# Kernel optimization log

Hardware: AMD Instinct MI355X
Metric: run time of the kernel (lower is better)

The kernel has to match this reference:

```python
import jax, jax.numpy as jnp
import numpy as np

B, L, E = 128, 512, 128
NUM_Q, NUM_C, DIFF = 10000, 300, 100


def _lin(k, fan_in, fan_out):
    kw, kb = jax.random.split(k)
    s = 1.0 / np.sqrt(fan_in)
    W = jax.random.uniform(kw, (fan_in, fan_out), jnp.float32, -s, s)
    b = jax.random.uniform(kb, (fan_out,), jnp.float32, -s, s)
    return W, b


def setup_inputs() -> dict:
    key = jax.random.key(0)
    ks = jax.random.split(key, 24)
    inp = {
        "q": jax.random.randint(ks[0], (B, L), 0, NUM_Q),
        "c": jax.random.randint(ks[1], (B, L), 0, NUM_C),
        "sd": jax.random.randint(ks[2], (B, L), 0, DIFF + 99),
        "qd": jax.random.randint(ks[3], (B, L), 0, DIFF + 99),
        "a": jax.random.randint(ks[4], (B, L), 0, 2 * NUM_Q + 1),
        "qshft": jax.random.randint(ks[5], (B, L), 0, NUM_Q),
        "cshft": jax.random.randint(ks[6], (B, L), 0, NUM_C),
        "sdshft": jax.random.randint(ks[7], (B, L), 0, DIFF + 99),
        "qdshft": jax.random.randint(ks[8], (B, L), 0, DIFF + 99),
        "knowledge": jax.random.normal(ks[9], (1, E), jnp.float32) * 0.1,
        "q_tab": jax.random.normal(ks[10], (NUM_Q + 1, E), jnp.float32),
        "c_tab": jax.random.normal(ks[11], (NUM_C + 1, E), jnp.float32),
        "sd_tab": jax.random.normal(ks[12], (DIFF + 100, E), jnp.float32),
        "qd_tab": jax.random.normal(ks[13], (DIFF + 100, E), jnp.float32),
        "a_tab": jax.random.normal(ks[14], (2 * NUM_Q + 2, E), jnp.float32),
    }
    for name, fan_in, ki in [("1", 4 * E, 15), ("2", E, 16), ("3", E, 17),
                             ("4", 2 * E, 18), ("5", 2 * E, 19), ("6", 4 * E, 20)]:
        W, b = _lin(ks[ki], fan_in, E)
        inp[f"W{name}"], inp[f"b{name}"] = W, b
    Wf, bf = _lin(ks[21], E, 10)
    inp["Wf"], inp["bf"] = Wf, bf
    return inp


def reference(q, c, sd, qd, a, qshft, cshft, sdshft, qdshft,
              knowledge, q_tab, c_tab, sd_tab, qd_tab, a_tab,
              W1, b1, W2, b2, W3, b3, W4, b4, W5, b5, W6, b6, Wf, bf):
    # Embedding lookups  [B, L, E]
    q_e, c_e = q_tab[q], c_tab[c]
    sd_e, qd_e = sd_tab[sd], qd_tab[qd]
    a_e = a_tab[a]
    # input_data = linear_1(cat(q,c,sd,qd))  [B, L, E]
    inp = jnp.concatenate([q_e, c_e, sd_e, qd_e], -1) @ W1 + b1
    # (target_data in the torch code is dead: never used for the output)

    k0 = jnp.broadcast_to(knowledge, (q.shape[0], knowledge.shape[1]))  # [B, E]

    def step(k, xs):
        x, sd1, a1, qd1 = xs  # each [B, E]
        qq = x - k
        SDFt = jax.nn.sigmoid(qq @ W2 + b2) * jnp.tanh(qq @ W3 + b3)  # dropout=eval
        xa = jnp.concatenate([SDFt, a1], -1)
        PKAt = jax.nn.sigmoid(xa @ W4 + b4) * jnp.tanh(xa @ W5 + b5)
        ins = jnp.concatenate([k, a1, sd1, qd1], -1)
        gK = jax.nn.sigmoid(ins @ W6 + b6)
        k_new = gK * k + (1.0 - gK) * PKAt
        return k_new, k_new @ Wf + bf

    xs = (jnp.swapaxes(inp, 0, 1), jnp.swapaxes(sd_e, 0, 1),
          jnp.swapaxes(a_e, 0, 1), jnp.swapaxes(qd_e, 0, 1))  # [L, B, E]
    _, logits = jax.lax.scan(step, k0, xs)  # [L, B, 10]
    return jax.nn.sigmoid(jnp.swapaxes(logits, 0, 1))  # [B, L, 10]
```

## Files before the change

### kernel.cpp

```cpp
#include <hip/hip_runtime.h>
#include <hip/hip_bf16.h>
#include <stdint.h>

#define E_DIM 128
#define L_SEQ 512
#define B_SZ  128

typedef _Float16 h2 __attribute__((ext_vector_type(2)));
typedef _Float16 f16x8 __attribute__((ext_vector_type(8)));
typedef float f32x4 __attribute__((ext_vector_type(4)));

constexpr size_t SZ_W12 = 512 * 128 * 4;
constexpr size_t SZ_TQ  = 10001 * 128 * 4;
constexpr size_t SZ_TC  = 301 * 128 * 4;
constexpr size_t SZ_TS  = 200 * 128 * 4;
constexpr size_t SZ_TA  = 20002 * 128 * 4;

constexpr size_t OFF_W12  = 0;
constexpr size_t OFF_W13  = OFF_W12 + SZ_W12;
constexpr size_t OFF_BV2  = OFF_W13 + SZ_W12;
constexpr size_t OFF_BV3  = OFF_BV2 + 512;
constexpr size_t OFF_TQ2  = OFF_BV3 + 512;
constexpr size_t OFF_TQ3  = OFF_TQ2 + SZ_TQ;
constexpr size_t OFF_TC2  = OFF_TQ3 + SZ_TQ;
constexpr size_t OFF_TC3  = OFF_TC2 + SZ_TC;
constexpr size_t OFF_TSD2 = OFF_TC3 + SZ_TC;
constexpr size_t OFF_TSD3 = OFF_TSD2 + SZ_TS;
constexpr size_t OFF_TSD6 = OFF_TSD3 + SZ_TS;
constexpr size_t OFF_TQD2 = OFF_TSD6 + SZ_TS;
constexpr size_t OFF_TQD3 = OFF_TQD2 + SZ_TS;
constexpr size_t OFF_TQD6 = OFF_TQD3 + SZ_TS;
constexpr size_t OFF_TA4  = OFF_TQD6 + SZ_TS;
constexpr size_t OFF_TA5  = OFF_TA4 + SZ_TA;
constexpr size_t OFF_TA6  = OFF_TA5 + SZ_TA;
constexpr size_t OFF_K    = OFF_TA6 + SZ_TA;

__device__ __forceinline__ float fdot2f(unsigned int a, unsigned int b, float c) {
#if __has_builtin(__builtin_amdgcn_fdot2)
  return __builtin_amdgcn_fdot2(__builtin_bit_cast(h2, a), __builtin_bit_cast(h2, b), c, false);
#else
  h2 x = __builtin_bit_cast(h2, a), y = __builtin_bit_cast(h2, b);
  return c + (float)x[0] * (float)y[0] + (float)x[1] * (float)y[1];
#endif
}

__device__ __forceinline__ unsigned int packh2(float a, float b) {
  h2 v; v[0] = (_Float16)a; v[1] = (_Float16)b;
  return __builtin_bit_cast(unsigned int, v);
}

__device__ __forceinline__ float fsig(float x) {
  float t = __builtin_amdgcn_exp2f(-1.4426950408889634f * x);
  return __builtin_amdgcn_rcpf(1.0f + t);
}
__device__ __forceinline__ float ftanh(float x) {
  float t = __builtin_amdgcn_exp2f(2.8853900817779268f * x);
  return 1.0f - 2.0f * __builtin_amdgcn_rcpf(t + 1.0f);
}

#define BARRIER_RAW() asm volatile("s_waitcnt lgkmcnt(0)\n\ts_barrier" ::: "memory")

__global__ __launch_bounds__(256, 2) void prepA_kernel(
    const float* __restrict__ W1, const float* __restrict__ W2, const float* __restrict__ W3,
    const float* __restrict__ b1, const float* __restrict__ b2, const float* __restrict__ b3,
    char* __restrict__ ws) {
  float* W12 = (float*)(ws + OFF_W12);
  float* W13 = (float*)(ws + OFF_W13);
  float* bv2 = (float*)(ws + OFF_BV2);
  float* bv3 = (float*)(ws + OFF_BV3);
  const int blk = blockIdx.x, tid = threadIdx.x;
  if (blk < 512) {
    const int m = blk >> 8;
    const int rp = blk & 255;
    const float* M = m ? W3 : W2;
    float* dst = m ? W13 : W12;
    const int rr = tid >> 7, j = tid & 127;
    const int r = rp * 2 + rr;
    __shared__ float rowL[2][128];
    rowL[rr][j] = W1[r * 128 + j];
    __syncthreads();
    float acc = 0.0f;
#pragma unroll 8
    for (int t = 0; t < 128; t++) acc += rowL[rr][t] * M[t * 128 + j];
    dst[r * 128 + j] = acc;
  } else if (tid < 128) {
    float a2 = b2[tid], a3 = b3[tid];
    for (int t = 0; t < 128; t++) {
      float bb = b1[t];
      a2 += bb * W2[t * 128 + tid];
      a3 += bb * W3[t * 128 + tid];
    }
    bv2[tid] = a2;
    bv3[tid] = a3;
  }
}

__global__ __launch_bounds__(256, 2) void gemm_tab1_kernel(
    const float* __restrict__ q_tab, const float* __restrict__ c_tab,
    const float* __restrict__ sd_tab, const float* __restrict__ qd_tab,
    const float* __restrict__ a_tab,
    const float* __restrict__ W4, const float* __restrict__ W5, const float* __restrict__ W6,
    const float* __restrict__ b4, const float* __restrict__ b5, const float* __restrict__ b6,
    char* __restrict__ ws) {
  __shared__ _Float16 BT[128][136];
  __shared__ _Float16 At[32][136];
  __shared__ float biasL[128];

  const float* W12 = (const float*)(ws + OFF_W12);
  const float* W13 = (const float*)(ws + OFF_W13);
  const float* bv2f = (const float*)(ws + OFF_BV2);
  const float* bv3f = (const float*)(ws + OFF_BV3);

  const int bid = blockIdx.x, tid = threadIdx.x;
  const int wv = tid >> 6, ln = tid & 63;

  int task, rb;
  if      (bid < 79)  { task = 0;  rb = bid; }
  else if (bid < 158) { task = 1;  rb = bid - 79; }
  else if (bid < 161) { task = 2;  rb = bid - 158; }
  else if (bid < 164) { task = 3;  rb = bid - 161; }
  else if (bid < 166) { task = 4;  rb = bid - 164; }
  else if (bid < 168) { task = 5;  rb = bid - 166; }
  else if (bid < 170) { task = 6;  rb = bid - 168; }
  else if (bid < 172) { task = 7;  rb = bid - 170; }
  else if (bid < 174) { task = 8;  rb = bid - 172; }
  else if (bid < 176) { task = 9;  rb = bid - 174; }
  else if (bid < 333) { task = 10; rb = bid - 176; }
  else if (bid < 490) { task = 11; rb = bid - 333; }
  else                { task = 12; rb = bid - 490; }

  const float* src; int rows; const float* Bsrc; const float* bias; float* dst;
  switch (task) {
    case 0:  src = q_tab;  rows = 10001; Bsrc = W12;            bias = bv2f;   dst = (float*)(ws + OFF_TQ2);  break;
    case 1:  src = q_tab;  rows = 10001; Bsrc = W13;            bias = bv3f;   dst = (float*)(ws + OFF_TQ3);  break;
    case 2:  src = c_tab;  rows = 301;   Bsrc = W12 + 128*128;  bias = nullptr; dst = (float*)(ws + OFF_TC2);  break;
    case 3:  src = c_tab;  rows = 301;   Bsrc = W13 + 128*128;  bias = nullptr; dst = (float*)(ws + OFF_TC3);  break;
    case 4:  src = sd_tab; rows = 200;   Bsrc = W12 + 256*128;  bias = nullptr; dst = (float*)(ws + OFF_TSD2); break;
    case 5:  src = sd_tab; rows = 200;   Bsrc = W13 + 256*128;  bias = nullptr; dst = (float*)(ws + OFF_TSD3); break;
    case 6:  src = sd_tab; rows = 200;   Bsrc = W6  + 256*128;  bias = nullptr; dst = (float*)(ws + OFF_TSD6); break;
    case 7:  src = qd_tab; rows = 200;   Bsrc = W12 + 384*128;  bias = nullptr; dst = (float*)(ws + OFF_TQD2); break;
    case 8:  src = qd_tab; rows = 200;   Bsrc = W13 + 384*128;  bias = nullptr; dst = (float*)(ws + OFF_TQD3); break;
    case 9:  src = qd_tab; rows = 200;   Bsrc = W6  + 384*128;  bias = nullptr; dst = (float*)(ws + OFF_TQD6); break;
    case 10: src = a_tab;  rows = 20002; Bsrc = W4  + 128*128;  bias = b4;     dst = (float*)(ws + OFF_TA4);  break;
    case 11: src = a_tab;  rows = 20002; Bsrc = W5  + 128*128;  bias = b5;     dst = (float*)(ws + OFF_TA5);  break;
    default: src = a_tab;  rows = 20002; Bsrc = W6  + 128*128;  bias = b6;     dst = (float*)(ws + OFF_TA6);  break;
  }

#pragma unroll
  for (int r = 0; r < 8; r++) {
    const int k = (tid >> 4) + r * 16;
    const int j0 = (tid & 15) * 8;
    float4 v0 = *(const float4*)(Bsrc + k * 128 + j0);
    float4 v1 = *(const float4*)(Bsrc + k * 128 + j0 + 4);
    BT[j0 + 0][k] = (_Float16)v0.x; BT[j0 + 1][k] = (_Float16)v0.y;
    BT[j0 + 2][k] = (_Float16)v0.z; BT[j0 + 3][k] = (_Float16)v0.w;
    BT[j0 + 4][k] = (_Float16)v1.x; BT[j0 + 5][k] = (_Float16)v1.y;
    BT[j0 + 6][k] = (_Float16)v1.z; BT[j0 + 7][k] = (_Float16)v1.w;
  }
  if (tid < 128) biasL[tid] = bias ? bias[tid] : 0.0f;
  __syncthreads();

  f16x8 bfr[2][4];
#pragma unroll
  for (int ct = 0; ct < 2; ct++)
#pragma unroll
    for (int kt = 0; kt < 4; kt++) {
      const int col = wv * 32 + ct * 16 + (ln & 15);
      const int k = kt * 32 + (ln >> 4) * 8;
      bfr[ct][kt] = *(const f16x8*)&BT[col][k];
    }
  float bvl[2] = { biasL[wv * 32 + (ln & 15)], biasL[wv * 32 + 16 + (ln & 15)] };

  const int row_base = rb * 128;
  for (int ch = 0; ch < 4; ch++) {
    const int row0 = row_base + ch * 32;
    {
      const int r = tid >> 3, cb = (tid & 7) * 16;
      int sr = row0 + r; if (sr >= rows) sr = rows - 1;
      const float4* s4 = (const float4*)(src + (size_t)sr * 128 + cb);
      float4 v0 = s4[0], v1 = s4[1], v2 = s4[2], v3 = s4[3];
      f16x8 lo, hi;
      lo[0] = (_Float16)v0.x; lo[1] = (_Float16)v0.y; lo[2] = (_Float16)v0.z; lo[3] = (_Float16)v0.w;
      lo[4] = (_Float16)v1.x; lo[5] = (_Float16)v1.y; lo[6] = (_Float16)v1.z; lo[7] = (_Float16)v1.w;
      hi[0] = (_Float16)v2.x; hi[1] = (_Float16)v2.y; hi[2] = (_Float16)v2.z; hi[3] = (_Float16)v2.w;
      hi[4] = (_Float16)v3.x; hi[5] = (_Float16)v3.y; hi[6] = (_Float16)v3.z; hi[7] = (_Float16)v3.w;
      *(f16x8*)&At[r][cb] = lo;
      *(f16x8*)&At[r][cb + 8] = hi;
    }
    __syncthreads();
    f16x8 af[2][4];
#pragma unroll
    for (int rt = 0; rt < 2; rt++)
#pragma unroll
      for (int kt = 0; kt < 4; kt++) {
        const int row = rt * 16 + (ln & 15);
        const int k = kt * 32 + (ln >> 4) * 8;
        af[rt][kt] = *(const f16x8*)&At[row][k];
      }
    f32x4 acc[2][2];
#pragma unroll
    for (int rt = 0; rt < 2; rt++)
#pragma unroll
      for (int ct = 0; ct < 2; ct++) acc[rt][ct] = (f32x4){0.f, 0.f, 0.f, 0.f};
#pragma unroll
    for (int kt = 0; kt < 4; kt++)
#pragma unroll
      for (int ct = 0; ct < 2; ct++)
#pragma unroll
        for (int rt = 0; rt < 2; rt++)
          acc[rt][ct] = __builtin_amdgcn_mfma_f32_16x16x32_f16(af[rt][kt], bfr[ct][kt], acc[rt][ct], 0, 0, 0);
#pragma unroll
    for (int ct = 0; ct < 2; ct++) {
      const int col = wv * 32 + ct * 16 + (ln & 15);
      const float bv = bvl[ct];
#pragma unroll
      for (int rt = 0; rt < 2; rt++)
#pragma unroll
        for (int e = 0; e < 4; e++) {
          const int row = row0 + rt * 16 + (ln >> 4) * 4 + e;
          if (row < rows) dst[(size_t)row * 128 + col] = acc[rt][ct][e] + bv;
        }
    }
    __syncthreads();
  }
}


#define PREFETCH(S, P) do {                                                   \
    int _s = (S);                                                             \
    int _qi = idxb[g][0][_s], _ci = idxb[g][1][_s], _si = idxb[g][2][_s];     \
    int _di = idxb[g][3][_s], _ai = idxb[g][4][_s];                           \
    P##q2 = Tq2[_qi * 128 + j]; P##q3 = Tq3[_qi * 128 + j];                   \
    P##c2 = Tc2[_ci * 128 + j]; P##c3 = Tc3[_ci * 128 + j];                   \
    P##s2 = Ts2[_si * 128 + j]; P##s3 = Ts3[_si * 128 + j];                   \
    P##s6 = Ts6[_si * 128 + j];                                               \
    P##d2 = Td2[_di * 128 + j]; P##d3 = Td3[_di * 128 + j];                   \
    P##d6 = Td6[_di * 128 + j];                                               \
    P##a4 = Ta4[_ai * 128 + j]; P##a5 = Ta5[_ai * 128 + j];                   \
    P##a6 = Ta6[_ai * 128 + j];                                               \
  } while (0)

#define SCAN_STEP(P, S2, L) do {                                              \
    float u2a = 0.f, u2b = 0.f, u3a = 0.f, u3b = 0.f, u6a = 0.f, u6b = 0.f;   \
    {                                                                         \
      const uint4* kp4 = ((const uint4*)kpair[g]) + 8 * h;                    \
      _Pragma("unroll")                                                       \
      for (int i = 0; i < 8; i++) {                                           \
        uint4 kv = kp4[i];                                                    \
        u2a = fdot2f(kv.x, w2h[4 * i + 0], u2a);                              \
        u3a = fdot2f(kv.x, w3h[4 * i + 0], u3a);                              \
        u6a = fdot2f(kv.x, w6h[4 * i + 0], u6a);                              \
        u2b = fdot2f(kv.y, w2h[4 * i + 1], u2b);                              \
        u3b = fdot2f(kv.y, w3h[4 * i + 1], u3b);                              \
        u6b = fdot2f(kv.y, w6h[4 * i + 1], u6b);                              \
        u2a = fdot2f(kv.z, w2h[4 * i + 2], u2a);                              \
        u3a = fdot2f(kv.z, w3h[4 * i + 2], u3a);                              \
        u6a = fdot2f(kv.z, w6h[4 * i + 2], u6a);                              \
        u2b = fdot2f(kv.w, w2h[4 * i + 3], u2b);                              \
        u3b = fdot2f(kv.w, w3h[4 * i + 3], u3b);                              \
        u6b = fdot2f(kv.w, w6h[4 * i + 3], u6b);                              \
      }                                                                       \
    }                                                                         \
    float U2p = u2a + u2b, U3p = u3a + u3b, U6p = u6a + u6b;                  \
    U2p += __shfl_xor(U2p, 32);                                               \
    U3p += __shfl_xor(U3p, 32);                                               \
    U6p += __shfl_xor(U6p, 32);                                               \
    float U2 = (P##q2 + P##c2 + P##s2 + P##d2) - U2p;                         \
    float U3 = (P##q3 + P##c3 + P##s3 + P##d3) - U3p;                         \
    float U6 = (P##a6 + P##s6 + P##d6) + U6p;                                 \
    float sdft = fsig(U2) * ftanh(U3);                                        \
    float g_ = fsig(U6);                                                      \
    if (!h) ((_Float16*)sdfp[g])[j] = (_Float16)sdft;                         \
    BARRIER_RAW();                                    \
    float u4a = 0.f, u4b = 0.f, u5a = 0.f, u5b = 0.f;                         \
    {                                                                         \
      const uint4* sp4 = ((const uint4*)sdfp[g]) + 8 * h;                     \
      _Pragma("unroll")                                                       \
      for (int i = 0; i < 8; i++) {                                           \
        uint4 sv = sp4[i];                                                    \
        u4a = fdot2f(sv.x, w4h[4 * i + 0], u4a);                              \
        u5a = fdot2f(sv.x, w5h[4 * i + 0], u5a);                              \
        u4b = fdot2f(sv.y, w4h[4 * i + 1], u4b);                              \
        u5b = fdot2f(sv.y, w5h[4 * i + 1], u5b);                              \
        u4a = fdot2f(sv.z, w4h[4 * i + 2], u4a);                              \
        u5a = fdot2f(sv.z, w5h[4 * i + 2], u5a);                              \
        u4b = fdot2f(sv.w, w4h[4 * i + 3], u4b);                              \
        u5b = fdot2f(sv.w, w5h[4 * i + 3], u5b);                              \
      }                                                                       \
    }                                                                         \
    float U4p = u4a + u4b, U5p = u5a + u5b;                                   \
    U4p += __shfl_xor(U4p, 32);                                               \
    U5p += __shfl_xor(U5p, 32);                                               \
    float pk = fsig(U4p + P##a4) * ftanh(U5p + P##a5);                        \
    k = g_ * k + (1.0f - g_) * pk;                                            \
    if (h) ((_Float16*)kpair[g])[j] = (_Float16)k;                            \
    if (!h) Kout[((size_t)(base + (L))) * 128 + j] = k;                       \
    PREFETCH(S2, P);                                                          \
    BARRIER_RAW();                                       \
  } while (0)

__global__ __launch_bounds__(512, 2) void scan_kernel(
    const int* __restrict__ q, const int* __restrict__ c, const int* __restrict__ sd,
    const int* __restrict__ qd, const int* __restrict__ a,
    const float* __restrict__ knowledge,
    const float* __restrict__ W2, const float* __restrict__ W3, const float* __restrict__ W4,
    const float* __restrict__ W5, const float* __restrict__ W6,
    char* __restrict__ ws) {
  const int tid = threadIdx.x;
  const int g = tid >> 8;
  const int t256 = tid & 255;
  const int ln = tid & 63;
  const int wvl = (t256 >> 6);
  const int j = (wvl << 5) | (ln & 31);
  const int h = ln >> 5;
  const int b = (blockIdx.x << 1) | g;
  const int base = b * L_SEQ;

  const float* Tq2 = (const float*)(ws + OFF_TQ2);
  const float* Tq3 = (const float*)(ws + OFF_TQ3);
  const float* Tc2 = (const float*)(ws + OFF_TC2);
  const float* Tc3 = (const float*)(ws + OFF_TC3);
  const float* Ts2 = (const float*)(ws + OFF_TSD2);
  const float* Ts3 = (const float*)(ws + OFF_TSD3);
  const float* Ts6 = (const float*)(ws + OFF_TSD6);
  const float* Td2 = (const float*)(ws + OFF_TQD2);
  const float* Td3 = (const float*)(ws + OFF_TQD3);
  const float* Td6 = (const float*)(ws + OFF_TQD6);
  const float* Ta4 = (const float*)(ws + OFF_TA4);
  const float* Ta5 = (const float*)(ws + OFF_TA5);
  const float* Ta6 = (const float*)(ws + OFF_TA6);
  float* Kout = (float*)(ws + OFF_K);

  __shared__ int idxb[2][5][L_SEQ];
  __shared__ __align__(16) unsigned int kpair[2][64];
  __shared__ __align__(16) unsigned int sdfp[2][64];

  idxb[g][0][t256] = q[base + t256];  idxb[g][0][t256 + 256] = q[base + t256 + 256];
  idxb[g][1][t256] = c[base + t256];  idxb[g][1][t256 + 256] = c[base + t256 + 256];
  idxb[g][2][t256] = sd[base + t256]; idxb[g][2][t256 + 256] = sd[base + t256 + 256];
  idxb[g][3][t256] = qd[base + t256]; idxb[g][3][t256 + 256] = qd[base + t256 + 256];
  idxb[g][4][t256] = a[base + t256];  idxb[g][4][t256 + 256] = a[base + t256 + 256];

  unsigned int w2h[32], w3h[32], w6h[32], w4h[32], w5h[32];
  const int t0 = h * 64;
#pragma unroll
  for (int p = 0; p < 32; p++) {
    w2h[p] = packh2(W2[(t0 + 2 * p) * 128 + j], W2[(t0 + 2 * p + 1) * 128 + j]);
    w3h[p] = packh2(W3[(t0 + 2 * p) * 128 + j], W3[(t0 + 2 * p + 1) * 128 + j]);
    w6h[p] = packh2(W6[(t0 + 2 * p) * 128 + j], W6[(t0 + 2 * p + 1) * 128 + j]);
    w4h[p] = packh2(W4[(t0 + 2 * p) * 128 + j], W4[(t0 + 2 * p + 1) * 128 + j]);
    w5h[p] = packh2(W5[(t0 + 2 * p) * 128 + j], W5[(t0 + 2 * p + 1) * 128 + j]);
  }

  float k = knowledge[j];
  if (h) ((_Float16*)kpair[g])[j] = (_Float16)k;
  __syncthreads();

  float gAq2, gAq3, gAc2, gAc3, gAs2, gAs3, gAs6, gAd2, gAd3, gAd6, gAa4, gAa5, gAa6;
  float gBq2, gBq3, gBc2, gBc3, gBs2, gBs3, gBs6, gBd2, gBd3, gBd6, gBa4, gBa5, gBa6;
  PREFETCH(0, gA);
  PREFETCH(1, gB);

#pragma unroll 1
  for (int m = 0; m < L_SEQ / 2; m++) {
    const int l0 = 2 * m;
    const int s2 = (l0 + 2 < L_SEQ) ? (l0 + 2) : (L_SEQ - 1);
    const int s3 = (l0 + 3 < L_SEQ) ? (l0 + 3) : (L_SEQ - 1);
    SCAN_STEP(gA, s2, l0);
    SCAN_STEP(gB, s3, l0 + 1);
  }
}

__global__ __launch_bounds__(256, 2) void logits_kernel(
    const float* __restrict__ Wf, const float* __restrict__ bf,
    const char* __restrict__ ws, float* __restrict__ out) {
  __shared__ float WfL[1280];
  __shared__ float bfL[10];
  const int tid = threadIdx.x;
  for (int i = tid; i < 1280; i += 256) WfL[i] = Wf[i];
  if (tid < 10) bfL[tid] = bf[tid];
  __syncthreads();
  const float* K = (const float*)(ws + OFF_K);
  const int nrows = B_SZ * L_SEQ;
  for (int r = blockIdx.x * 256 + tid; r < nrows; r += gridDim.x * 256) {
    const float4* kr = (const float4*)(K + (size_t)r * 128);
    float acc[10];
#pragma unroll
    for (int i = 0; i < 10; i++) acc[i] = bfL[i];
#pragma unroll
    for (int t4 = 0; t4 < 32; t4++) {
      float4 v = kr[t4];
#pragma unroll
      for (int i = 0; i < 10; i++)
        acc[i] += v.x * WfL[(4 * t4 + 0) * 10 + i] + v.y * WfL[(4 * t4 + 1) * 10 + i] +
                  v.z * WfL[(4 * t4 + 2) * 10 + i] + v.w * WfL[(4 * t4 + 3) * 10 + i];
    }
    float* o = out + (size_t)r * 10;
#pragma unroll
    for (int i = 0; i < 10; i++) o[i] = fsig(acc[i]);
  }
}

extern "C" void kernel_launch(void* const* d_in, const int* in_sizes, int n_in,
                              void* d_out, int out_size, void* d_ws, size_t ws_size,
                              hipStream_t stream) {
  const int* q  = (const int*)d_in[0];
  const int* c  = (const int*)d_in[1];
  const int* sd = (const int*)d_in[2];
  const int* qd = (const int*)d_in[3];
  const int* a  = (const int*)d_in[4];
  const float* knowledge = (const float*)d_in[9];
  const float* q_tab  = (const float*)d_in[10];
  const float* c_tab  = (const float*)d_in[11];
  const float* sd_tab = (const float*)d_in[12];
  const float* qd_tab = (const float*)d_in[13];
  const float* a_tab  = (const float*)d_in[14];
  const float* W1 = (const float*)d_in[15];
  const float* b1 = (const float*)d_in[16];
  const float* W2 = (const float*)d_in[17];
  const float* b2 = (const float*)d_in[18];
  const float* W3 = (const float*)d_in[19];
  const float* b3 = (const float*)d_in[20];
  const float* W4 = (const float*)d_in[21];
  const float* b4 = (const float*)d_in[22];
  const float* W5 = (const float*)d_in[23];
  const float* b5 = (const float*)d_in[24];
  const float* W6 = (const float*)d_in[25];
  const float* b6 = (const float*)d_in[26];
  const float* Wf = (const float*)d_in[27];
  const float* bf = (const float*)d_in[28];
  char* ws = (char*)d_ws;
  float* out = (float*)d_out;

  prepA_kernel<<<513, 256, 0, stream>>>(W1, W2, W3, b1, b2, b3, ws);
  gemm_tab1_kernel<<<647, 256, 0, stream>>>(q_tab, c_tab, sd_tab, qd_tab, a_tab,
                                            W4, W5, W6, b4, b5, b6, ws);
  scan_kernel<<<B_SZ / 2, 512, 0, stream>>>(q, c, sd, qd, a, knowledge, W2, W3, W4, W5, W6, ws);
  logits_kernel<<<256, 256, 0, stream>>>(Wf, bf, ws, out);
}
```

Measured before the change: 883.6 us.

## Interleave precomputed projection tables for vector gathers in scan

The precomputed per-embedding projection tables are now written interleaved (q/c pairs, sd/qd quads, a4/a5 pairs), so each scan step issues six vector gathers instead of thirteen scalar loads. Gather indices are made wave-uniform with readfirstlane so the address math can live in scalar registers. The scan kernel's launch bounds drop to one block per SM, which gives the compiler more registers but may lower occupancy. The precompute stores become strided, which could cost some write efficiency.

New measurement: 888.2 us. No clear change (+0.5%).

```diff
diff --git a/kernel.cpp b/kernel.cpp
--- a/kernel.cpp
+++ b/kernel.cpp
@@ -10,30 +10,26 @@
 typedef _Float16 f16x8 __attribute__((ext_vector_type(8)));
 typedef float f32x4 __attribute__((ext_vector_type(4)));
 
-constexpr size_t SZ_W12 = 512 * 128 * 4;
-constexpr size_t SZ_TQ  = 10001 * 128 * 4;
-constexpr size_t SZ_TC  = 301 * 128 * 4;
-constexpr size_t SZ_TS  = 200 * 128 * 4;
-constexpr size_t SZ_TA  = 20002 * 128 * 4;
+constexpr size_t SZ_W12  = 512 * 128 * 4;
+constexpr size_t SZ_TQ   = (size_t)10001 * 128 * 2 * 4;
+constexpr size_t SZ_TC   = (size_t)301 * 128 * 2 * 4;
+constexpr size_t SZ_TSD  = (size_t)200 * 128 * 4 * 4;
+constexpr size_t SZ_TQD  = (size_t)200 * 128 * 4 * 4;
+constexpr size_t SZ_TA45 = (size_t)20002 * 128 * 2 * 4;
+constexpr size_t SZ_TA6  = (size_t)20002 * 128 * 4;
+constexpr size_t SZ_K    = (size_t)B_SZ * L_SEQ * 128 * 4;
 
 constexpr size_t OFF_W12  = 0;
 constexpr size_t OFF_W13  = OFF_W12 + SZ_W12;
 constexpr size_t OFF_BV2  = OFF_W13 + SZ_W12;
 constexpr size_t OFF_BV3  = OFF_BV2 + 512;
-constexpr size_t OFF_TQ2  = OFF_BV3 + 512;
-constexpr size_t OFF_TQ3  = OFF_TQ2 + SZ_TQ;
-constexpr size_t OFF_TC2  = OFF_TQ3 + SZ_TQ;
-constexpr size_t OFF_TC3  = OFF_TC2 + SZ_TC;
-constexpr size_t OFF_TSD2 = OFF_TC3 + SZ_TC;
-constexpr size_t OFF_TSD3 = OFF_TSD2 + SZ_TS;
-constexpr size_t OFF_TSD6 = OFF_TSD3 + SZ_TS;
-constexpr size_t OFF_TQD2 = OFF_TSD6 + SZ_TS;
-constexpr size_t OFF_TQD3 = OFF_TQD2 + SZ_TS;
-constexpr size_t OFF_TQD6 = OFF_TQD3 + SZ_TS;
-constexpr size_t OFF_TA4  = OFF_TQD6 + SZ_TS;
-constexpr size_t OFF_TA5  = OFF_TA4 + SZ_TA;
-constexpr size_t OFF_TA6  = OFF_TA5 + SZ_TA;
-constexpr size_t OFF_K    = OFF_TA6 + SZ_TA;
+constexpr size_t OFF_TQ   = OFF_BV3 + 512;
+constexpr size_t OFF_TC   = OFF_TQ + SZ_TQ;
+constexpr size_t OFF_TSD  = OFF_TC + SZ_TC;
+constexpr size_t OFF_TQD  = OFF_TSD + SZ_TSD;
+constexpr size_t OFF_TA45 = OFF_TQD + SZ_TQD;
+constexpr size_t OFF_TA6  = OFF_TA45 + SZ_TA45;
+constexpr size_t OFF_K    = OFF_TA6 + SZ_TA6;
 
 __device__ __forceinline__ float fdot2f(unsigned int a, unsigned int b, float c) {
 #if __has_builtin(__builtin_amdgcn_fdot2)
@@ -129,21 +125,22 @@
   else if (bid < 490) { task = 11; rb = bid - 333; }
   else                { task = 12; rb = bid - 490; }
 
-  const float* src; int rows; const float* Bsrc; const float* bias; float* dst;
+  const float* src; int rows; const float* Bsrc; const float* bias;
+  float* dst; int STR, ILV, SLOT;
   switch (task) {
-    case 0:  src = q_tab;  rows = 10001; Bsrc = W12;            bias = bv2f;   dst = (float*)(ws + OFF_TQ2);  break;
-    case 1:  src = q_tab;  rows = 10001; Bsrc = W13;            bias = bv3f;   dst = (float*)(ws + OFF_TQ3);  break;
-    case 2:  src = c_tab;  rows = 301;   Bsrc = W12 + 128*128;  bias = nullptr; dst = (float*)(ws + OFF_TC2);  break;
-    case 3:  src = c_tab;  rows = 301;   Bsrc = W13 + 128*128;  bias = nullptr; dst = (float*)(ws + OFF_TC3);  break;
-    case 4:  src = sd_tab; rows = 200;   Bsrc = W12 + 256*128;  bias = nullptr; dst = (float*)(ws + OFF_TSD2); break;
-    case 5:  src = sd_tab; rows = 200;   Bsrc = W13 + 256*128;  bias = nullptr; dst = (float*)(ws + OFF_TSD3); break;
-    case 6:  src = sd_tab; rows = 200;   Bsrc = W6  + 256*128;  bias = nullptr; dst = (float*)(ws + OFF_TSD6); break;
-    case 7:  src = qd_tab; rows = 200;   Bsrc = W12 + 384*128;  bias = nullptr; dst = (float*)(ws + OFF_TQD2); break;
-    case 8:  src = qd_tab; rows = 200;   Bsrc = W13 + 384*128;  bias = nullptr; dst = (float*)(ws + OFF_TQD3); break;
-    case 9:  src = qd_tab; rows = 200;   Bsrc = W6  + 384*128;  bias = nullptr; dst = (float*)(ws + OFF_TQD6); break;
-    case 10: src = a_tab;  rows = 20002; Bsrc = W4  + 128*128;  bias = b4;     dst = (float*)(ws + OFF_TA4);  break;
-    case 11: src = a_tab;  rows = 20002; Bsrc = W5  + 128*128;  bias = b5;     dst = (float*)(ws + OFF_TA5);  break;
-    default: src = a_tab;  rows = 20002; Bsrc = W6  + 128*128;  bias = b6;     dst = (float*)(ws + OFF_TA6);  break;
+    case 0:  src = q_tab;  rows = 10001; Bsrc = W12;           bias = bv2f;    dst = (float*)(ws + OFF_TQ);   STR = 256; ILV = 2; SLOT = 0; break;
+    case 1:  src = q_tab;  rows = 10001; Bsrc = W13;           bias = bv3f;    dst = (float*)(ws + OFF_TQ);   STR = 256; ILV = 2; SLOT = 1; break;
+    case 2:  src = c_tab;  rows = 301;   Bsrc = W12 + 128*128; bias = nullptr; dst = (float*)(ws + OFF_TC);   STR = 256; ILV = 2; SLOT = 0; break;
+    case 3:  src = c_tab;  rows = 301;   Bsrc = W13 + 128*128; bias = nullptr; dst = (float*)(ws + OFF_TC);   STR = 256; ILV = 2; SLOT = 1; break;
+    case 4:  src = sd_tab; rows = 200;   Bsrc = W12 + 256*128; bias = nullptr; dst = (float*)(ws + OFF_TSD);  STR = 512; ILV = 4; SLOT = 0; break;
+    case 5:  src = sd_tab; rows = 200;   Bsrc = W13 + 256*128; bias = nullptr; dst = (float*)(ws + OFF_TSD);  STR = 512; ILV = 4; SLOT = 1; break;
+    case 6:  src = sd_tab; rows = 200;   Bsrc = W6  + 256*128; bias = nullptr; dst = (float*)(ws + OFF_TSD);  STR = 512; ILV = 4; SLOT = 2; break;
+    case 7:  src = qd_tab; rows = 200;   Bsrc = W12 + 384*128; bias = nullptr; dst = (float*)(ws + OFF_TQD);  STR = 512; ILV = 4; SLOT = 0; break;
+    case 8:  src = qd_tab; rows = 200;   Bsrc = W13 + 384*128; bias = nullptr; dst = (float*)(ws + OFF_TQD);  STR = 512; ILV = 4; SLOT = 1; break;
+    case 9:  src = qd_tab; rows = 200;   Bsrc = W6  + 384*128; bias = nullptr; dst = (float*)(ws + OFF_TQD);  STR = 512; ILV = 4; SLOT = 2; break;
+    case 10: src = a_tab;  rows = 20002; Bsrc = W4  + 128*128; bias = b4;      dst = (float*)(ws + OFF_TA45); STR = 256; ILV = 2; SLOT = 0; break;
+    case 11: src = a_tab;  rows = 20002; Bsrc = W5  + 128*128; bias = b5;      dst = (float*)(ws + OFF_TA45); STR = 256; ILV = 2; SLOT = 1; break;
+    default: src = a_tab;  rows = 20002; Bsrc = W6  + 128*128; bias = b6;      dst = (float*)(ws + OFF_TA6);  STR = 128; ILV = 1; SLOT = 0; break;
   }
 
 #pragma unroll
@@ -218,7 +215,7 @@
 #pragma unroll
         for (int e = 0; e < 4; e++) {
           const int row = row0 + rt * 16 + (ln >> 4) * 4 + e;
-          if (row < rows) dst[(size_t)row * 128 + col] = acc[rt][ct][e] + bv;
+          if (row < rows) dst[(size_t)row * STR + col * ILV + SLOT] = acc[rt][ct][e] + bv;
         }
     }
     __syncthreads();
@@ -228,16 +225,17 @@
 
 #define PREFETCH(S, P) do {                                                   \
     int _s = (S);                                                             \
-    int _qi = idxb[g][0][_s], _ci = idxb[g][1][_s], _si = idxb[g][2][_s];     \
-    int _di = idxb[g][3][_s], _ai = idxb[g][4][_s];                           \
-    P##q2 = Tq2[_qi * 128 + j]; P##q3 = Tq3[_qi * 128 + j];                   \
-    P##c2 = Tc2[_ci * 128 + j]; P##c3 = Tc3[_ci * 128 + j];                   \
-    P##s2 = Ts2[_si * 128 + j]; P##s3 = Ts3[_si * 128 + j];                   \
-    P##s6 = Ts6[_si * 128 + j];                                               \
-    P##d2 = Td2[_di * 128 + j]; P##d3 = Td3[_di * 128 + j];                   \
-    P##d6 = Td6[_di * 128 + j];                                               \
-    P##a4 = Ta4[_ai * 128 + j]; P##a5 = Ta5[_ai * 128 + j];                   \
-    P##a6 = Ta6[_ai * 128 + j];                                               \
+    int _qi = __builtin_amdgcn_readfirstlane(idxb[g][0][_s]);                 \
+    int _ci = __builtin_amdgcn_readfirstlane(idxb[g][1][_s]);                 \
+    int _si = __builtin_amdgcn_readfirstlane(idxb[g][2][_s]);                 \
+    int _di = __builtin_amdgcn_readfirstlane(idxb[g][3][_s]);                 \
+    int _ai = __builtin_amdgcn_readfirstlane(idxb[g][4][_s]);                 \
+    P##q  = *(const float2*)(Tq   + ((size_t)_qi << 8) + (j << 1));           \
+    P##c  = *(const float2*)(Tc   + ((size_t)_ci << 8) + (j << 1));           \
+    P##s  = *(const float4*)(Ts   + ((size_t)_si << 9) + (j << 2));           \
+    P##d  = *(const float4*)(Td   + ((size_t)_di << 9) + (j << 2));           \
+    P##a  = *(const float2*)(Ta45 + ((size_t)_ai << 8) + (j << 1));           \
+    P##a6 = Ta6[((size_t)_ai << 7) + j];                                      \
   } while (0)
 
 #define SCAN_STEP(P, S2, L) do {                                              \
@@ -265,9 +263,9 @@
     U2p += __shfl_xor(U2p, 32);                                               \
     U3p += __shfl_xor(U3p, 32);                                               \
     U6p += __shfl_xor(U6p, 32);                                               \
-    float U2 = (P##q2 + P##c2 + P##s2 + P##d2) - U2p;                         \
-    float U3 = (P##q3 + P##c3 + P##s3 + P##d3) - U3p;                         \
-    float U6 = (P##a6 + P##s6 + P##d6) + U6p;                                 \
+    float U2 = (P##q.x + P##c.x + P##s.x + P##d.x) - U2p;                     \
+    float U3 = (P##q.y + P##c.y + P##s.y + P##d.y) - U3p;                     \
+    float U6 = (P##a6 + P##s.z + P##d.z) + U6p;                               \
     float sdft = fsig(U2) * ftanh(U3);                                        \
     float g_ = fsig(U6);                                                      \
     if (!h) ((_Float16*)sdfp[g])[j] = (_Float16)sdft;                         \
@@ -291,7 +289,7 @@
     float U4p = u4a + u4b, U5p = u5a + u5b;                                   \
     U4p += __shfl_xor(U4p, 32);                                               \
     U5p += __shfl_xor(U5p, 32);                                               \
-    float pk = fsig(U4p + P##a4) * ftanh(U5p + P##a5);                        \
+    float pk = fsig(U4p + P##a.x) * ftanh(U5p + P##a.y);                      \
     k = g_ * k + (1.0f - g_) * pk;                                            \
     if (h) ((_Float16*)kpair[g])[j] = (_Float16)k;                            \
     if (!h) Kout[((size_t)(base + (L))) * 128 + j] = k;                       \
@@ -299,7 +297,7 @@
     BARRIER_RAW();                                       \
   } while (0)
 
-__global__ __launch_bounds__(512, 2) void scan_kernel(
+__global__ __launch_bounds__(512, 1) void scan_kernel(
     const int* __restrict__ q, const int* __restrict__ c, const int* __restrict__ sd,
     const int* __restrict__ qd, const int* __restrict__ a,
     const float* __restrict__ knowledge,
@@ -316,19 +314,12 @@
   const int b = (blockIdx.x << 1) | g;
   const int base = b * L_SEQ;
 
-  const float* Tq2 = (const float*)(ws + OFF_TQ2);
-  const float* Tq3 = (const float*)(ws + OFF_TQ3);
-  const float* Tc2 = (const float*)(ws + OFF_TC2);
-  const float* Tc3 = (const float*)(ws + OFF_TC3);
-  const float* Ts2 = (const float*)(ws + OFF_TSD2);
-  const float* Ts3 = (const float*)(ws + OFF_TSD3);
-  const float* Ts6 = (const float*)(ws + OFF_TSD6);
-  const float* Td2 = (const float*)(ws + OFF_TQD2);
-  const float* Td3 = (const float*)(ws + OFF_TQD3);
-  const float* Td6 = (const float*)(ws + OFF_TQD6);
-  const float* Ta4 = (const float*)(ws + OFF_TA4);
-  const float* Ta5 = (const float*)(ws + OFF_TA5);
-  const float* Ta6 = (const float*)(ws + OFF_TA6);
+  const float* Tq   = (const float*)(ws + OFF_TQ);
+  const float* Tc   = (const float*)(ws + OFF_TC);
+  const float* Ts   = (const float*)(ws + OFF_TSD);
+  const float* Td   = (const float*)(ws + OFF_TQD);
+  const float* Ta45 = (const float*)(ws + OFF_TA45);
+  const float* Ta6  = (const float*)(ws + OFF_TA6);
   float* Kout = (float*)(ws + OFF_K);
 
   __shared__ int idxb[2][5][L_SEQ];
@@ -356,8 +347,8 @@
   if (h) ((_Float16*)kpair[g])[j] = (_Float16)k;
   __syncthreads();
 
-  float gAq2, gAq3, gAc2, gAc3, gAs2, gAs3, gAs6, gAd2, gAd3, gAd6, gAa4, gAa5, gAa6;
-  float gBq2, gBq3, gBc2, gBc3, gBs2, gBs3, gBs6, gBd2, gBd3, gBd6, gBa4, gBa5, gBa6;
+  float2 gAq, gAc, gAa; float4 gAs, gAd; float gAa6;
+  float2 gBq, gBc, gBa; float4 gBs, gBd; float gBa6;
   PREFETCH(0, gA);
   PREFETCH(1, gB);
 
```
